# Kernel tuning notes

Hardware: AMD Instinct MI355X
Metric: run time of the kernel (lower is better)

The kernel has to match this reference:

```python
import jax, jax.numpy as jnp
import numpy as np


def _gcn_conv(x, src, dst, num_nodes, W, b):
    """PyG GCNConv: add self-loops, symmetric normalization, scatter-add, bias."""
    h = x @ W  # [N, F_out]
    # degree over destination nodes (all edge weights are 1, incl. self-loops)
    deg = jax.ops.segment_sum(jnp.ones_like(dst, dtype=h.dtype), dst,
                              num_segments=num_nodes)
    deg_inv_sqrt = jnp.where(deg > 0, jax.lax.rsqrt(deg), 0.0)
    norm = deg_inv_sqrt[src] * deg_inv_sqrt[dst]  # [E+N]
    msg = h[src] * norm[:, None]                  # gather + scale
    out = jax.ops.segment_sum(msg, dst, num_segments=num_nodes)  # scatter-add
    return out + b


def setup_inputs() -> dict:
    key = jax.random.key(0)
    k_x, k_e, k_w1, k_w2 = jax.random.split(key, 4)
    N, E, F = 50000, 800000, 128
    x = jax.random.normal(k_x, (N, F), dtype=jnp.float32)
    edge_index = jax.random.randint(k_e, (2, E), 0, N, dtype=jnp.int64)
    scale = 1.0 / np.sqrt(F)
    W1 = jax.random.normal(k_w1, (F, F), dtype=jnp.float32) * scale
    b1 = jnp.zeros((F,), dtype=jnp.float32)
    W2 = jax.random.normal(k_w2, (F, F), dtype=jnp.float32) * scale
    b2 = jnp.zeros((F,), dtype=jnp.float32)
    return {"x": x, "edge_index": edge_index, "W1": W1, "b1": b1,
            "W2": W2, "b2": b2}


def reference(x, edge_index, W1, b1, W2, b2):
    num_nodes = x.shape[0]
    loops = jnp.arange(num_nodes, dtype=edge_index.dtype)
    src = jnp.concatenate([edge_index[0], loops])
    dst = jnp.concatenate([edge_index[1], loops])
    # layer 1: GCNConv -> Identity norm -> relu -> dropout(eval=identity)
    h = jax.nn.relu(_gcn_conv(x, src, dst, num_nodes, W1, b1))
    # layer 2 (last_activation=True, so relu again)
    out = jax.nn.relu(_gcn_conv(h, src, dst, num_nodes, W2, b2))
    return out
```

## Files before the change

kernel.cpp:

```cpp
#include <hip/hip_runtime.h>
#include <hip/hip_bf16.h>

#define CDIV(a,b) (((a)+(b)-1)/(b))

typedef __bf16 bf16x8 __attribute__((ext_vector_type(8)));
typedef float  f32x4  __attribute__((ext_vector_type(4)));

union Frag16 { uint4 u; bf16x8 f; unsigned short s[8]; };
union Pack8  { unsigned short s[4]; uint2 u; };

__device__ __forceinline__ unsigned short f2bf(float f) {
    unsigned u = __float_as_uint(f);
    return (unsigned short)((u + 0x7fff + ((u >> 16) & 1)) >> 16);
}
__device__ __forceinline__ float bf2f(unsigned short s) {
    return __uint_as_float(((unsigned)s) << 16);
}

__device__ __forceinline__ int load_src(const int* e, int f, int E, int i) {
    return f ? e[i] : e[2 * i];
}
__device__ __forceinline__ int load_dst(const int* e, int f, int E, int i) {
    return f ? e[E + i] : e[2 * (E + i)];
}

__global__ __launch_bounds__(256) void prep_kernel(const float* __restrict__ W1,
                                                   const float* __restrict__ W2,
                                                   unsigned short* __restrict__ Wf1h,
                                                   unsigned short* __restrict__ Wf1l,
                                                   unsigned short* __restrict__ Wf2h,
                                                   unsigned short* __restrict__ Wf2l,
                                                   const int* __restrict__ edges,
                                                   int* __restrict__ flag, int E,
                                                   int4* __restrict__ zero_base, int Z4) {
    int tid = threadIdx.x;
    if (blockIdx.x == 2) {
        if (tid == 0) *flag = 0;
        __syncthreads();
        int n = min(E, 4096);
        int found = 0;
        for (int j = tid; j < n; j += 256) found |= (edges[2 * j + 1] != 0);
        if (found) *flag = 1;
        return;
    }
    if (blockIdx.x >= 3) {
        int idx = (blockIdx.x - 3) * 256 + tid;
        if (idx < Z4) zero_base[idx] = make_int4(0, 0, 0, 0);
        return;
    }
    const float* W = (blockIdx.x == 0) ? W1 : W2;
    unsigned short* Wfh = (blockIdx.x == 0) ? Wf1h : Wf2h;
    unsigned short* Wfl = (blockIdx.x == 0) ? Wf1l : Wf2l;
    #pragma unroll
    for (int it = 0; it < 8; ++it) {
        int c = it * 256 + tid;
        int ntk = c >> 6;
        int lane = c & 63;
        int ks = ntk & 3;
        int ntile = ntk >> 2;
        int quad = lane >> 4, nlo = lane & 15;
        int n = ntile * 16 + nlo;
        Frag16 h, l;
        #pragma unroll
        for (int j = 0; j < 8; ++j) {
            float w = W[(ks * 32 + quad * 8 + j) * 128 + n];
            h.s[j] = f2bf(w);
            float rr = w - bf2f(h.s[j]);
            l.s[j] = f2bf(rr);
        }
        *(uint4*)(Wfh + (size_t)c * 8) = h.u;
        *(uint4*)(Wfl + (size_t)c * 8) = l.u;
    }
}

__device__ __forceinline__ void gemm_body(const float* __restrict__ X,
                                          const unsigned short* __restrict__ Wfh,
                                          const unsigned short* __restrict__ Wfl,
                                          unsigned short* __restrict__ out16,
                                          int N, int blk,
                                          unsigned short (*Xh)[136],
                                          unsigned short (*Xl)[136]) {
    int tid = threadIdx.x;
    int row0 = blk * 64;
    #pragma unroll
    for (int it = 0; it < 8; ++it) {
        int f = it * 256 + tid;
        int r = f >> 5, c4 = f & 31;
        float4 v = make_float4(0.f, 0.f, 0.f, 0.f);
        int gr = row0 + r;
        if (gr < N) v = *(const float4*)(X + (size_t)gr * 128 + c4 * 4);
        float vv[4] = {v.x, v.y, v.z, v.w};
        Pack8 h, l;
        #pragma unroll
        for (int j = 0; j < 4; ++j) {
            h.s[j] = f2bf(vv[j]);
            float rr = vv[j] - bf2f(h.s[j]);
            l.s[j] = f2bf(rr);
        }
        *(uint2*)(&Xh[r][c4 * 4]) = h.u;
        *(uint2*)(&Xl[r][c4 * 4]) = l.u;
    }
    __syncthreads();

    int lane = tid & 63;
    int wv = tid >> 6;
    int quad = lane >> 4, nlo = lane & 15;
    f32x4 acc[8];
    #pragma unroll
    for (int t = 0; t < 8; ++t) acc[t] = (f32x4){0.f, 0.f, 0.f, 0.f};

    #pragma unroll
    for (int ks = 0; ks < 4; ++ks) {
        int kcol = ks * 32 + quad * 8;
        Frag16 xh, xl;
        xh.u = *(const uint4*)(&Xh[wv * 16 + nlo][kcol]);
        xl.u = *(const uint4*)(&Xl[wv * 16 + nlo][kcol]);
        #pragma unroll
        for (int t = 0; t < 8; ++t) {
            size_t cidx = ((size_t)(t * 4 + ks) * 64 + lane) * 8;
            Frag16 wh, wl;
            wh.u = *(const uint4*)(Wfh + cidx);
            wl.u = *(const uint4*)(Wfl + cidx);
            acc[t] = __builtin_amdgcn_mfma_f32_16x16x32_bf16(xh.f, wh.f, acc[t], 0, 0, 0);
            acc[t] = __builtin_amdgcn_mfma_f32_16x16x32_bf16(xh.f, wl.f, acc[t], 0, 0, 0);
            acc[t] = __builtin_amdgcn_mfma_f32_16x16x32_bf16(xl.f, wh.f, acc[t], 0, 0, 0);
        }
    }
    #pragma unroll
    for (int rg = 0; rg < 4; ++rg) {
        int gr = row0 + wv * 16 + quad * 4 + rg;
        if (gr < N) {
            #pragma unroll
            for (int t = 0; t < 8; ++t)
                out16[(size_t)gr * 128 + t * 16 + nlo] = f2bf(acc[t][rg]);
        }
    }
}

__global__ __launch_bounds__(256) void fat_kernel(const float* __restrict__ X,
                                                  const unsigned short* __restrict__ Wfh,
                                                  const unsigned short* __restrict__ Wfl,
                                                  unsigned short* __restrict__ out16,
                                                  int N, int Ggemm,
                                                  const int* __restrict__ edges,
                                                  const int* __restrict__ flag,
                                                  int* __restrict__ counts_sh,
                                                  int* __restrict__ rank, int E) {
    __shared__ unsigned short Xh[64][136];
    __shared__ unsigned short Xl[64][136];
    if (blockIdx.x < (unsigned)Ggemm) {
        gemm_body(X, Wfh, Wfl, out16, N, blockIdx.x, Xh, Xl);
        return;
    }
    int e = (blockIdx.x - Ggemm) * 256 + threadIdx.x;
    if (e >= E) return;
    int f = *flag;
    int d = load_dst(edges, f, E, e);
    int s = blockIdx.x & 7;
    int r = atomicAdd(&counts_sh[s * N + d], 1);
    rank[e] = (r << 3) | s;
}

__global__ __launch_bounds__(256) void merge_dis_kernel(int* __restrict__ counts_sh,
                                                        int* __restrict__ counts,
                                                        float* __restrict__ dis,
                                                        int* __restrict__ bsum, int N) {
    __shared__ int red[4];
    int tid = threadIdx.x;
    int bs = 0;
    #pragma unroll
    for (int j = 0; j < 4; ++j) {
        int d = blockIdx.x * 1024 + j * 256 + tid;
        if (d < N) {
            int run = 0;
            #pragma unroll
            for (int s = 0; s < 8; ++s) {
                int v = counts_sh[s * N + d];
                counts_sh[s * N + d] = run;
                run += v;
            }
            counts[d] = run;
            dis[d] = rsqrtf((float)(run + 1));
            bs += run;
        }
    }
    #pragma unroll
    for (int off = 32; off >= 1; off >>= 1) bs += __shfl_down(bs, off, 64);
    if ((tid & 63) == 0) red[tid >> 6] = bs;
    __syncthreads();
    if (tid == 0) bsum[blockIdx.x] = red[0] + red[1] + red[2] + red[3];
}

__global__ void scan2_kernel(const int* __restrict__ bsum, int* __restrict__ boff,
                             int B, int* __restrict__ row_ptr, int N, int E) {
    int lane = threadIdx.x;
    int carry = 0;
    for (int base = 0; base < B; base += 64) {
        int i = base + lane;
        int v = (i < B) ? bsum[i] : 0;
        int x = v;
        #pragma unroll
        for (int off = 1; off < 64; off <<= 1) {
            int t = __shfl_up(x, off, 64);
            if (lane >= off) x += t;
        }
        if (i < B) boff[i] = carry + x - v;
        carry += __shfl(x, 63, 64);
    }
    if (lane == 0) row_ptr[N] = E;
}

__global__ __launch_bounds__(256) void scan3_kernel(const int* __restrict__ counts,
                                                    const int* __restrict__ boff,
                                                    int* __restrict__ row_ptr, int N) {
    __shared__ int wsum[4];
    int tid = threadIdx.x;
    int lane = tid & 63, wv = tid >> 6;
    int base = blockIdx.x * 1024 + tid * 4;
    int c[4];
    #pragma unroll
    for (int j = 0; j < 4; ++j) c[j] = (base + j < N) ? counts[base + j] : 0;
    int tsum = c[0] + c[1] + c[2] + c[3];
    int x = tsum;
    #pragma unroll
    for (int off = 1; off < 64; off <<= 1) {
        int t = __shfl_up(x, off, 64);
        if (lane >= off) x += t;
    }
    int texcl = x - tsum;
    if (lane == 63) wsum[wv] = x;
    __syncthreads();
    int woff = 0;
    for (int w = 0; w < wv; ++w) woff += wsum[w];
    int off0 = boff[blockIdx.x] + woff + texcl;
    int run = 0;
    #pragma unroll
    for (int j = 0; j < 4; ++j) {
        if (base + j < N) row_ptr[base + j] = off0 + run;
        run += c[j];
    }
}

__global__ void fill_kernel(const int* __restrict__ edges, const int* __restrict__ flag,
                            const int* __restrict__ row_ptr, const int* __restrict__ rank,
                            const int* __restrict__ counts_sh,
                            const float* __restrict__ dis, int2* __restrict__ edata,
                            int E, int N) {
    int e = blockIdx.x * blockDim.x + threadIdx.x;
    if (e >= E) return;
    int f = *flag;
    int s = load_src(edges, f, E, e);
    int d = load_dst(edges, f, E, e);
    int rk = rank[e];
    int sh = rk & 7;
    int pos = row_ptr[d] + counts_sh[sh * N + d] + (rk >> 3);
    edata[pos] = make_int2(s, __float_as_int(dis[s]));
}

__global__ __launch_bounds__(1024) void agg1_fused_kernel(
        const unsigned short* __restrict__ A16,
        const int* __restrict__ row_ptr,
        const int2* __restrict__ edata,
        const float* __restrict__ dis,
        const float* __restrict__ bias,
        const unsigned short* __restrict__ Wfh,
        const unsigned short* __restrict__ Wfl,
        unsigned short* __restrict__ H1out, int N) {
    __shared__ unsigned short Hl[16][128];
    int wv = threadIdx.x >> 6;
    int lane = threadIdx.x & 63;
    int wid = blockIdx.x * 16 + wv;
    if (wid < N) {
        const ushort2* H2 = (const ushort2*)A16;
        float dd = dis[wid];
        ushort2 hv = H2[(size_t)wid * 64 + lane];
        float wself = dd * dd;
        float2 acc = make_float2(bf2f(hv.x) * wself, bf2f(hv.y) * wself);
        int e0 = __builtin_amdgcn_readfirstlane(row_ptr[wid]);
        int e1 = __builtin_amdgcn_readfirstlane(row_ptr[wid + 1]);
        for (int e = e0; e < e1; e += 8) {
            int rem = e1 - e;
            int   sj[8];
            float wj[8];
            #pragma unroll
            for (int j = 0; j < 8; ++j) {
                bool valid = j < rem;
                int2 ed = edata[valid ? e + j : e];
                sj[j] = ed.x;
                wj[j] = valid ? __int_as_float(ed.y) * dd : 0.f;
            }
            ushort2 aj[8];
            #pragma unroll
            for (int j = 0; j < 8; ++j)
                aj[j] = H2[(size_t)sj[j] * 64 + lane];
            #pragma unroll
            for (int j = 0; j < 8; ++j) {
                acc.x += bf2f(aj[j].x) * wj[j];
                acc.y += bf2f(aj[j].y) * wj[j];
            }
        }
        float2 b = ((const float2*)bias)[lane];
        float ox = fmaxf(acc.x + b.x, 0.f);
        float oy = fmaxf(acc.y + b.y, 0.f);
        int c = (lane * 2) ^ ((wv & 7) << 3);
        *(ushort2*)(&Hl[wv][c]) = make_ushort2(f2bf(ox), f2bf(oy));
    }
    __syncthreads();
    if (wv >= 8) return;
    int quad = lane >> 4, nlo = lane & 15;
    f32x4 acc = (f32x4){0.f, 0.f, 0.f, 0.f};
    #pragma unroll
    for (int ks = 0; ks < 4; ++ks) {
        int cb = (ks * 32 + quad * 8) ^ ((nlo & 7) << 3);
        Frag16 xa, wh, wl;
        xa.u = *(const uint4*)(&Hl[nlo][cb]);
        size_t cidx = ((size_t)(wv * 4 + ks) * 64 + lane) * 8;
        wh.u = *(const uint4*)(Wfh + cidx);
        wl.u = *(const uint4*)(Wfl + cidx);
        acc = __builtin_amdgcn_mfma_f32_16x16x32_bf16(xa.f, wh.f, acc, 0, 0, 0);
        acc = __builtin_amdgcn_mfma_f32_16x16x32_bf16(xa.f, wl.f, acc, 0, 0, 0);
    }
    #pragma unroll
    for (int rg = 0; rg < 4; ++rg) {
        int gr = blockIdx.x * 16 + quad * 4 + rg;
        if (gr < N)
            H1out[(size_t)gr * 128 + wv * 16 + nlo] = f2bf(acc[rg]);
    }
}

__global__ __launch_bounds__(256) void agg2_kernel(const unsigned short* __restrict__ H16,
                                                   const int* __restrict__ row_ptr,
                                                   const int2* __restrict__ edata,
                                                   const float* __restrict__ dis,
                                                   const float* __restrict__ bias,
                                                   float* __restrict__ outp, int N) {
    int wid = (blockIdx.x * blockDim.x + threadIdx.x) >> 6;
    int lane = threadIdx.x & 63;
    if (wid >= N) return;
    const ushort2* H2 = (const ushort2*)H16;
    float dd = dis[wid];
    ushort2 hv = H2[(size_t)wid * 64 + lane];
    float wself = dd * dd;
    float2 acc = make_float2(bf2f(hv.x) * wself, bf2f(hv.y) * wself);
    int e0 = __builtin_amdgcn_readfirstlane(row_ptr[wid]);
    int e1 = __builtin_amdgcn_readfirstlane(row_ptr[wid + 1]);
    for (int e = e0; e < e1; e += 8) {
        int rem = e1 - e;
        int   sj[8];
        float wj[8];
        #pragma unroll
        for (int j = 0; j < 8; ++j) {
            bool valid = j < rem;
            int2 ed = edata[valid ? e + j : e];
            sj[j] = ed.x;
            wj[j] = valid ? __int_as_float(ed.y) * dd : 0.f;
        }
        ushort2 aj[8];
        #pragma unroll
        for (int j = 0; j < 8; ++j)
            aj[j] = H2[(size_t)sj[j] * 64 + lane];
        #pragma unroll
        for (int j = 0; j < 8; ++j) {
            acc.x += bf2f(aj[j].x) * wj[j];
            acc.y += bf2f(aj[j].y) * wj[j];
        }
    }
    float2 b = ((const float2*)bias)[lane];
    float ox = fmaxf(acc.x + b.x, 0.f);
    float oy = fmaxf(acc.y + b.y, 0.f);
    ((float2*)outp)[(size_t)wid * 64 + lane] = make_float2(ox, oy);
}

extern "C" void kernel_launch(void* const* d_in, const int* in_sizes, int n_in,
                              void* d_out, int out_size, void* d_ws, size_t ws_size,
                              hipStream_t stream) {
    const float* x    = (const float*)d_in[0];
    const int*  edges = (const int*)d_in[1];
    const float* W1   = (const float*)d_in[2];
    const float* b1   = (const float*)d_in[3];
    const float* W2   = (const float*)d_in[4];
    const float* b2   = (const float*)d_in[5];
    float* out = (float*)d_out;

    const int F = 128;
    const int N = in_sizes[0] / F;
    const int E = in_sizes[1] / 2;
    const int NB = CDIV(N, 1024);
    const int Ggemm = CDIV(N, 64);
    const int Gcount = CDIV(E, 256);

    #define AL4(v) (((v) + 3) & ~3)
    unsigned short* A16 = (unsigned short*)d_ws;
    unsigned short* H1  = A16 + (size_t)AL4(N * F);
    float* dis      = (float*)(H1 + (size_t)AL4(N * F));
    int*  counts    = (int*)(dis + AL4(N));
    int*  counts_sh = counts + AL4(N);
    int*  flag      = counts_sh + AL4(8 * N);
    int*  row_ptr   = flag + 4;
    int*  bsum      = row_ptr + AL4(N + 1);
    int*  boff      = bsum + 64;
    int*  rank      = boff + 64;
    int2* edata     = (int2*)(rank + AL4(E));
    unsigned short* Wf1h = (unsigned short*)(edata + E);
    unsigned short* Wf1l = Wf1h + 16384;
    unsigned short* Wf2h = Wf1l + 16384;
    unsigned short* Wf2l = Wf2h + 16384;

    const int Z4 = AL4(8 * N) / 4;
    const int Gprep = 3 + CDIV(Z4, 256);

    prep_kernel<<<Gprep, 256, 0, stream>>>(W1, W2, Wf1h, Wf1l, Wf2h, Wf2l,
                                           edges, flag, E, (int4*)counts_sh, Z4);
    fat_kernel<<<Ggemm + Gcount, 256, 0, stream>>>(x, Wf1h, Wf1l, A16, N, Ggemm,
                                                   edges, flag, counts_sh, rank, E);
    merge_dis_kernel<<<NB, 256, 0, stream>>>(counts_sh, counts, dis, bsum, N);
    scan2_kernel<<<1, 64, 0, stream>>>(bsum, boff, NB, row_ptr, N, E);
    scan3_kernel<<<NB, 256, 0, stream>>>(counts, boff, row_ptr, N);
    fill_kernel<<<Gcount, 256, 0, stream>>>(edges, flag, row_ptr, rank,
                                            counts_sh, dis, edata, E, N);

    agg1_fused_kernel<<<CDIV(N, 16), 1024, 0, stream>>>(A16, row_ptr, edata, dis,
                                                        b1, Wf2h, Wf2l, H1, N);
    agg2_kernel<<<CDIV(N * 64, 256), 256, 0, stream>>>(H1, row_ptr, edata, dis, b2, out, N);
}
```

Measured before the change: 217.2 us.

## Fuse merge and scan kernels via decoupled lookback; widen agg2 edge batch

Combines the merge, block-sum scan and row-pointer scan kernels into one kernel. Each block publishes its flagged block sum, and later blocks spin on those flags to compute their prefix offset, which removes two launches and the counts round-trip through memory. The bsum flags are zeroed by extending the prep kernel's clear region. Separately, agg2 now gathers 16 edges per iteration instead of 8 to keep more loads in flight, at the cost of more registers. The lookback relies on every earlier block being resident or finished, which holds for the small grid here (NB=49).

```diff
diff --git a/kernel.cpp b/kernel.cpp
--- a/kernel.cpp
+++ b/kernel.cpp
@@ -161,16 +161,25 @@
     rank[e] = (r << 3) | s;
 }
 
-__global__ __launch_bounds__(256) void merge_dis_kernel(int* __restrict__ counts_sh,
-                                                        int* __restrict__ counts,
-                                                        float* __restrict__ dis,
-                                                        int* __restrict__ bsum, int N) {
+#define BSUM_FLAG 0x40000000
+__global__ __launch_bounds__(256) void merge_scan_kernel(int* __restrict__ counts_sh,
+                                                         float* __restrict__ dis,
+                                                         int* __restrict__ bsum,
+                                                         int* __restrict__ row_ptr,
+                                                         int N, int E) {
     __shared__ int red[4];
+    __shared__ int wsum[4];
+    __shared__ int boff_sh;
     int tid = threadIdx.x;
+    int bid = blockIdx.x;
+    if (bid == 0 && tid == 0) row_ptr[N] = E;
+    int base = bid * 1024 + tid * 4;
+    int cnt[4];
     int bs = 0;
     #pragma unroll
     for (int j = 0; j < 4; ++j) {
-        int d = blockIdx.x * 1024 + j * 256 + tid;
+        int d = base + j;
+        cnt[j] = 0;
         if (d < N) {
             int run = 0;
             #pragma unroll
@@ -179,65 +188,56 @@
                 counts_sh[s * N + d] = run;
                 run += v;
             }
-            counts[d] = run;
+            cnt[j] = run;
             dis[d] = rsqrtf((float)(run + 1));
             bs += run;
         }
     }
-    #pragma unroll
-    for (int off = 32; off >= 1; off >>= 1) bs += __shfl_down(bs, off, 64);
-    if ((tid & 63) == 0) red[tid >> 6] = bs;
+    int t = bs;
+    #pragma unroll
+    for (int off = 32; off >= 1; off >>= 1) t += __shfl_down(t, off, 64);
+    if ((tid & 63) == 0) red[tid >> 6] = t;
     __syncthreads();
-    if (tid == 0) bsum[blockIdx.x] = red[0] + red[1] + red[2] + red[3];
-}
-
-__global__ void scan2_kernel(const int* __restrict__ bsum, int* __restrict__ boff,
-                             int B, int* __restrict__ row_ptr, int N, int E) {
-    int lane = threadIdx.x;
-    int carry = 0;
-    for (int base = 0; base < B; base += 64) {
-        int i = base + lane;
-        int v = (i < B) ? bsum[i] : 0;
-        int x = v;
-        #pragma unroll
-        for (int off = 1; off < 64; off <<= 1) {
-            int t = __shfl_up(x, off, 64);
-            if (lane >= off) x += t;
-        }
-        if (i < B) boff[i] = carry + x - v;
-        carry += __shfl(x, 63, 64);
-    }
-    if (lane == 0) row_ptr[N] = E;
-}
-
-__global__ __launch_bounds__(256) void scan3_kernel(const int* __restrict__ counts,
-                                                    const int* __restrict__ boff,
-                                                    int* __restrict__ row_ptr, int N) {
-    __shared__ int wsum[4];
-    int tid = threadIdx.x;
+    if (tid == 0) {
+        int total = red[0] + red[1] + red[2] + red[3];
+        __hip_atomic_store(&bsum[bid], total | BSUM_FLAG,
+                           __ATOMIC_RELEASE, __HIP_MEMORY_SCOPE_AGENT);
+    }
+    if (tid < 64) {
+        int sum = 0;
+        for (int p = tid; p < bid; p += 64) {
+            int v;
+            do {
+                v = __hip_atomic_load(&bsum[p], __ATOMIC_ACQUIRE,
+                                      __HIP_MEMORY_SCOPE_AGENT);
+                if (!(v & BSUM_FLAG)) __builtin_amdgcn_s_sleep(1);
+            } while (!(v & BSUM_FLAG));
+            sum += v & (BSUM_FLAG - 1);
+        }
+        #pragma unroll
+        for (int off = 32; off >= 1; off >>= 1) sum += __shfl_down(sum, off, 64);
+        if (tid == 0) boff_sh = sum;
+    }
+    __syncthreads();
     int lane = tid & 63, wv = tid >> 6;
-    int base = blockIdx.x * 1024 + tid * 4;
-    int c[4];
-    #pragma unroll
-    for (int j = 0; j < 4; ++j) c[j] = (base + j < N) ? counts[base + j] : 0;
-    int tsum = c[0] + c[1] + c[2] + c[3];
+    int tsum = cnt[0] + cnt[1] + cnt[2] + cnt[3];
     int x = tsum;
     #pragma unroll
     for (int off = 1; off < 64; off <<= 1) {
-        int t = __shfl_up(x, off, 64);
-        if (lane >= off) x += t;
+        int u = __shfl_up(x, off, 64);
+        if (lane >= off) x += u;
     }
     int texcl = x - tsum;
     if (lane == 63) wsum[wv] = x;
     __syncthreads();
     int woff = 0;
     for (int w = 0; w < wv; ++w) woff += wsum[w];
-    int off0 = boff[blockIdx.x] + woff + texcl;
+    int off0 = boff_sh + woff + texcl;
     int run = 0;
     #pragma unroll
     for (int j = 0; j < 4; ++j) {
         if (base + j < N) row_ptr[base + j] = off0 + run;
-        run += c[j];
+        run += cnt[j];
     }
 }
 
@@ -344,23 +344,23 @@
     float2 acc = make_float2(bf2f(hv.x) * wself, bf2f(hv.y) * wself);
     int e0 = __builtin_amdgcn_readfirstlane(row_ptr[wid]);
     int e1 = __builtin_amdgcn_readfirstlane(row_ptr[wid + 1]);
-    for (int e = e0; e < e1; e += 8) {
+    for (int e = e0; e < e1; e += 16) {
         int rem = e1 - e;
-        int   sj[8];
-        float wj[8];
-        #pragma unroll
-        for (int j = 0; j < 8; ++j) {
+        int   sj[16];
+        float wj[16];
+        #pragma unroll
+        for (int j = 0; j < 16; ++j) {
             bool valid = j < rem;
             int2 ed = edata[valid ? e + j : e];
             sj[j] = ed.x;
             wj[j] = valid ? __int_as_float(ed.y) * dd : 0.f;
         }
-        ushort2 aj[8];
-        #pragma unroll
-        for (int j = 0; j < 8; ++j)
+        ushort2 aj[16];
+        #pragma unroll
+        for (int j = 0; j < 16; ++j)
             aj[j] = H2[(size_t)sj[j] * 64 + lane];
         #pragma unroll
-        for (int j = 0; j < 8; ++j) {
+        for (int j = 0; j < 16; ++j) {
             acc.x += bf2f(aj[j].x) * wj[j];
             acc.y += bf2f(aj[j].y) * wj[j];
         }
@@ -393,29 +393,25 @@
     unsigned short* A16 = (unsigned short*)d_ws;
     unsigned short* H1  = A16 + (size_t)AL4(N * F);
     float* dis      = (float*)(H1 + (size_t)AL4(N * F));
-    int*  counts    = (int*)(dis + AL4(N));
-    int*  counts_sh = counts + AL4(N);
-    int*  flag      = counts_sh + AL4(8 * N);
+    int*  counts_sh = (int*)(dis + AL4(N));
+    int*  bsum      = counts_sh + AL4(8 * N);
+    int*  flag      = bsum + 64;
     int*  row_ptr   = flag + 4;
-    int*  bsum      = row_ptr + AL4(N + 1);
-    int*  boff      = bsum + 64;
-    int*  rank      = boff + 64;
+    int*  rank      = row_ptr + AL4(N + 1);
     int2* edata     = (int2*)(rank + AL4(E));
     unsigned short* Wf1h = (unsigned short*)(edata + E);
     unsigned short* Wf1l = Wf1h + 16384;
     unsigned short* Wf2h = Wf1l + 16384;
     unsigned short* Wf2l = Wf2h + 16384;
 
-    const int Z4 = AL4(8 * N) / 4;
+    const int Z4 = (AL4(8 * N) + 64) / 4;
     const int Gprep = 3 + CDIV(Z4, 256);
 
     prep_kernel<<<Gprep, 256, 0, stream>>>(W1, W2, Wf1h, Wf1l, Wf2h, Wf2l,
                                            edges, flag, E, (int4*)counts_sh, Z4);
     fat_kernel<<<Ggemm + Gcount, 256, 0, stream>>>(x, Wf1h, Wf1l, A16, N, Ggemm,
                                                    edges, flag, counts_sh, rank, E);
-    merge_dis_kernel<<<NB, 256, 0, stream>>>(counts_sh, counts, dis, bsum, N);
-    scan2_kernel<<<1, 64, 0, stream>>>(bsum, boff, NB, row_ptr, N, E);
-    scan3_kernel<<<NB, 256, 0, stream>>>(counts, boff, row_ptr, N);
+    merge_scan_kernel<<<NB, 256, 0, stream>>>(counts_sh, dis, bsum, row_ptr, N, E);
     fill_kernel<<<Gcount, 256, 0, stream>>>(edges, flag, row_ptr, rank,
                                             counts_sh, dis, edata, E, N);
 
```

Result: no change. 215.3 us, median of 2 (-0.9%).
